# Performance work log

Hardware: AMD Instinct MI355X
Metric: run time of the kernel (lower is better)

## Reference

```python
import jax, jax.numpy as jnp
import numpy as np

N_E = 1024
E_DIM = 256
TAU = 0.5
BETA = 0.25
LAMB = 0.1
EPS = 1e-10


def setup_inputs() -> dict:
    key = jax.random.key(0)
    k1, k2, k3 = jax.random.split(key, 3)
    z = jax.random.normal(k1, (16, 1024, E_DIM), dtype=jnp.float32)
    # kaiming-normal-initialized codebook (std = sqrt(2 / fan_in))
    emb = jax.random.normal(k2, (N_E, E_DIM), dtype=jnp.float32) * np.sqrt(2.0 / E_DIM)
    u = jax.random.uniform(k3, (16 * 1024, N_E), dtype=jnp.float32)
    return {"z": z, "emb": emb, "u": u}


def reference(z, emb, u):
    zf = z.reshape(-1, E_DIM)                                  # [N, e_dim]
    # squared euclidean distances to each code: ||z||^2 + ||e||^2 - 2 z.e
    d = (jnp.sum(zf * zf, axis=1, keepdims=True)
         + jnp.sum(emb * emb, axis=1)
         - 2.0 * jnp.matmul(zf, emb.T))                        # [N, n_e]
    # gumbel-softmax (hard, straight-through) on logits = -d
    g = -jnp.log(-jnp.log(u + EPS) + EPS)
    y_soft = jax.nn.softmax((-d + g) / TAU, axis=-1)
    idx = jnp.argmax(y_soft, axis=-1)
    y_hard = jax.nn.one_hot(idx, N_E, dtype=y_soft.dtype)
    probs = y_hard + y_soft - jax.lax.stop_gradient(y_soft)    # [N, n_e]
    z_q = jnp.matmul(probs, emb).reshape(z.shape)
    # orthogonality loss on the codebook gram matrix
    gram = jnp.matmul(emb, emb.T)
    ortho = jnp.mean((gram - jnp.eye(N_E, dtype=emb.dtype)) ** 2) / (N_E ** 2)
    emb_loss = jnp.mean((jax.lax.stop_gradient(z_q) - z) ** 2)
    commit = BETA * jnp.mean((z_q - jax.lax.stop_gradient(z)) ** 2)
    loss = emb_loss + BETA * commit + LAMB * ortho
    z_q_st = z + jax.lax.stop_gradient(z_q - z)
    e_mean = jnp.mean(probs, axis=0)
    perplexity = jnp.exp(-jnp.sum(e_mean * jnp.log(e_mean + EPS)))
    return loss, z_q_st, perplexity
```

## Files before the change

### kernel.cpp

```cpp
#include <hip/hip_runtime.h>
#include <math.h>
#include <stdint.h>


#define NROWS 16384
#define NE    1024
#define ED    256
#define EPSF  1e-10f
#define INV2048 4.8828125e-4f
#define BK 64

typedef _Float16 half_t;
typedef __attribute__((ext_vector_type(4))) _Float16 half4;
typedef __attribute__((ext_vector_type(8))) _Float16 half8;
typedef __attribute__((ext_vector_type(16))) float floatx16;
typedef unsigned long long u64;

__device__ __forceinline__ void gl_lds16(const half_t* g, half_t* l) {
    __builtin_amdgcn_global_load_lds(
        (const __attribute__((address_space(1))) uint32_t*)g,
        (__attribute__((address_space(3))) uint32_t*)l, 16, 0, 0);
}

__device__ __forceinline__ u64 packMax(float v, int code) {
    unsigned int b   = __float_as_uint(v);
    unsigned int key = (b & 0x80000000u) ? ~b : (b | 0x80000000u);
    return ((u64)key << 32) | (unsigned int)(NE - 1 - code);
}

__global__ __launch_bounds__(256) void vq_prep(
        const float* __restrict__ z, const float* __restrict__ emb,
        half_t* __restrict__ zh, half_t* __restrict__ zl,
        half_t* __restrict__ eh, half_t* __restrict__ el,
        float* __restrict__ enorm, u64* __restrict__ best,
        int* __restrict__ cnt, double* __restrict__ mse_acc,
        int* __restrict__ done_cnt)
{
    const int gid = blockIdx.x * 256 + threadIdx.x;
    const int ZQ4 = NROWS * ED / 4;
    if (gid < ZQ4) {
        const float4 v = ((const float4*)z)[gid];
        const float x[4] = {v.x, v.y, v.z, v.w};
        half4 h, l;
#pragma unroll
        for (int i = 0; i < 4; ++i) {
            const half_t hi = (half_t)x[i];
            h[i] = hi; l[i] = (half_t)((x[i] - (float)hi) * 2048.0f);
        }
        *(half4*)&zh[(size_t)gid * 4] = h;
        *(half4*)&zl[(size_t)gid * 4] = l;
    } else {
        const int eg = gid - ZQ4;
        const float4 v = ((const float4*)emb)[eg];
        const float x[4] = {v.x, v.y, v.z, v.w};
        half4 h, l;
#pragma unroll
        for (int i = 0; i < 4; ++i) {
            const half_t hi = (half_t)x[i];
            h[i] = hi; l[i] = (half_t)((x[i] - (float)hi) * 2048.0f);
        }
        *(half4*)&eh[(size_t)eg * 4] = h;
        *(half4*)&el[(size_t)eg * 4] = l;
        float s = v.x*v.x + v.y*v.y + v.z*v.z + v.w*v.w;
#pragma unroll
        for (int o = 32; o; o >>= 1) s += __shfl_down(s, o);
        if ((threadIdx.x & 63) == 0) enorm[eg >> 6] = s;
        if (eg < NROWS) best[eg] = 0ull;
        if (eg < NE)    cnt[eg]  = 0;
        if (eg == 0)  { *mse_acc = 0.0; *done_cnt = 0; }
    }
}

#define SCW 132
__global__ __launch_bounds__(256, 2) void vq_gemm(
        const half_t* __restrict__ zh, const half_t* __restrict__ zl,
        const half_t* __restrict__ eh, const half_t* __restrict__ el,
        const float* __restrict__ u, const float* __restrict__ enorm,
        u64* __restrict__ best)
{
    __shared__ __align__(16) char smem[128 * SCW * 4 + 2048];
    half_t* Ah = (half_t*)smem;
    half_t* Al = (half_t*)(smem + 16384);
    half_t* Bh = (half_t*)(smem + 32768);
    half_t* Bl = (half_t*)(smem + 49152);
    float (*Sc)[SCW] = (float(*)[SCW])smem;
    u64* parr = (u64*)(smem + 128 * SCW * 4);

    const int t    = threadIdx.x;
    const int w    = t >> 6;
    const int lane = t & 63;
    const int m0 = blockIdx.x * 128, n0 = blockIdx.y * 128;
    const int wm = (w >> 1) * 64,    wn = (w & 1) * 64;
    const int lrow = lane & 31;
    const int hw   = lane >> 5;

    floatx16 accH[2][2] = {};
    floatx16 accX[2][2] = {};

    for (int kc = 0; kc < ED; kc += BK) {
        __syncthreads();
#pragma unroll
        for (int it = 0; it < 4; ++it) {
            const int s   = it * 256 + t;
            const int row = s >> 3;
            const int c   = (s & 7) ^ (row & 7);
            const int ldsoff = (it * 256 + w * 64) * 8;
            const size_t ga = (size_t)(m0 + row) * ED + kc + c * 8;
            const size_t gb = (size_t)(n0 + row) * ED + kc + c * 8;
            gl_lds16(zh + ga, Ah + ldsoff);
            gl_lds16(zl + ga, Al + ldsoff);
            gl_lds16(eh + gb, Bh + ldsoff);
            gl_lds16(el + gb, Bl + ldsoff);
        }
        __syncthreads();
#pragma unroll
        for (int ks = 0; ks < BK / 16; ++ks) {
            const int cch = ks * 2 + hw;
            half8 ah[2], al[2], bh[2], bl[2];
#pragma unroll
            for (int i = 0; i < 2; ++i) {
                const int ar = wm + i * 32 + lrow;
                const int br = wn + i * 32 + lrow;
                const int sa = ar * 8 + (cch ^ (ar & 7));
                const int sb = br * 8 + (cch ^ (br & 7));
                ah[i] = *(const half8*)&Ah[sa * 8];
                al[i] = *(const half8*)&Al[sa * 8];
                bh[i] = *(const half8*)&Bh[sb * 8];
                bl[i] = *(const half8*)&Bl[sb * 8];
            }
#pragma unroll
            for (int i = 0; i < 2; ++i)
#pragma unroll
            for (int j = 0; j < 2; ++j) {
                accH[i][j] = __builtin_amdgcn_mfma_f32_32x32x16_f16(ah[i], bh[j], accH[i][j], 0, 0, 0);
                accX[i][j] = __builtin_amdgcn_mfma_f32_32x32x16_f16(ah[i], bl[j], accX[i][j], 0, 0, 0);
                accX[i][j] = __builtin_amdgcn_mfma_f32_32x32x16_f16(al[i], bh[j], accX[i][j], 0, 0, 0);
            }
        }
    }
    __syncthreads();

    const int   col0 = n0 + wn + lrow;
    const float en0  = enorm[col0];
    const float en1  = enorm[col0 + 32];
#pragma unroll
    for (int i = 0; i < 2; ++i) {
#pragma unroll
        for (int r = 0; r < 16; ++r) {
            const int lr = wm + i * 32 + (r & 3) + ((r >> 2) << 3) + (hw << 2);
            const size_t urow = (size_t)(m0 + lr) * NE;
            const float d0 = accH[i][0][r] + accX[i][0][r] * INV2048;
            const float d1 = accH[i][1][r] + accX[i][1][r] * INV2048;
            const float g0 = -__logf(-__logf(u[urow + col0] + EPSF) + EPSF);
            const float g1 = -__logf(-__logf(u[urow + col0 + 32] + EPSF) + EPSF);
            Sc[lr][wn + lrow]      = 2.f * d0 - en0 + g0;
            Sc[lr][wn + lrow + 32] = 2.f * d1 - en1 + g1;
        }
    }
    __syncthreads();

    {
        const int row = t >> 1;
        const int ch  = (t & 1) << 6;
        float bv = -1e38f; int bc = 0;
#pragma unroll
        for (int q = 0; q < 16; ++q) {
            const float4 v = *(const float4*)&Sc[row][ch + (q << 2)];
            const int c = n0 + ch + (q << 2);
            if (v.x > bv) { bv = v.x; bc = c; }
            if (v.y > bv) { bv = v.y; bc = c + 1; }
            if (v.z > bv) { bv = v.z; bc = c + 2; }
            if (v.w > bv) { bv = v.w; bc = c + 3; }
        }
        parr[t] = packMax(bv, bc);
    }
    __syncthreads();
    if (t < 128) {
        const u64 a = parr[t << 1], b = parr[(t << 1) + 1];
        atomicMax(&best[m0 + t], a > b ? a : b);
    }
}

__global__ __launch_bounds__(256) void vq_outfin(
        const float* __restrict__ z, const float* __restrict__ emb,
        const u64* __restrict__ best, int* __restrict__ cnt,
        double* __restrict__ mse_acc, int* __restrict__ done_cnt,
        float* __restrict__ out)
{
    __shared__ int    ridx[64];
    __shared__ float  redf[4];
    __shared__ double redd[4];
    __shared__ int    flag;
    const int t  = threadIdx.x;
    const int m0 = blockIdx.x * 64;

    if (t < 64) {
        const u64 p = best[m0 + t];
        const int code = NE - 1 - (int)(p & 0xFFFFFFFFu);
        ridx[t] = code;
        atomicAdd(&cnt[code], 1);
    }
    __syncthreads();

    float lmse = 0.f;
#pragma unroll
    for (int rr = 0; rr < 16; ++rr) {
        const int row = (rr << 2) + (t >> 6);
        const int d4  = (t & 63) << 2;
        const int j   = ridx[row];
        const size_t zb = (size_t)(m0 + row) * ED;
        const float4 zv = *(const float4*)&z[zb + d4];
        const float4 ev = *(const float4*)&emb[(size_t)j * ED + d4];
        const float zz[4] = {zv.x, zv.y, zv.z, zv.w};
        const float ee[4] = {ev.x, ev.y, ev.z, ev.w};
#pragma unroll
        for (int q = 0; q < 4; ++q) {
            const float df = ee[q] - zz[q];
            out[1 + zb + d4 + q] = zz[q] + df;
            lmse = fmaf(df, df, lmse);
        }
    }
#pragma unroll
    for (int o = 32; o; o >>= 1) lmse += __shfl_down(lmse, o);
    if ((t & 63) == 0) redf[t >> 6] = lmse;
    __syncthreads();
    if (t == 0) {
        atomicAdd(mse_acc, (double)(redf[0] + redf[1] + redf[2] + redf[3]));
        __threadfence();
        flag = (atomicAdd(done_cnt, 1) == NROWS / 64 - 1) ? 1 : 0;
    }
    __syncthreads();
    if (flag) {
        double s = 0.0;
#pragma unroll
        for (int q = 0; q < 4; ++q) {
            const int   c  = atomicAdd(&cnt[(q << 8) + t], 0);
            const float em = (float)c / (float)NROWS;
            s += (double)(em * logf(em + EPSF));
        }
#pragma unroll
        for (int o = 32; o; o >>= 1) s += __shfl_down(s, o);
        if ((t & 63) == 0) redd[t >> 6] = s;
        __syncthreads();
        if (t == 0) {
            const double tot = redd[0] + redd[1] + redd[2] + redd[3];
            const double mse = atomicAdd(mse_acc, 0.0) / (double)((size_t)NROWS * ED);
            out[0] = (float)(mse * 1.0625);
            out[1 + (size_t)NROWS * ED] = (float)exp(-tot);
        }
    }
}

extern "C" void kernel_launch(void* const* d_in, const int* in_sizes, int n_in,
                              void* d_out, int out_size, void* d_ws, size_t ws_size,
                              hipStream_t stream) {
    const float* z   = (const float*)d_in[0];
    const float* emb = (const float*)d_in[1];
    const float* u   = (const float*)d_in[2];
    float* out = (float*)d_out;

    double* mse_acc  = (double*)d_ws;
    int*    done_cnt = (int*)((char*)d_ws + 64);
    int*    cnt      = (int*)((char*)d_ws + 1024);
    float*  enorm    = (float*)((char*)d_ws + 5120);
    u64*    best     = (u64*)((char*)d_ws + 9216);
    const size_t small_end = 140288;

    const size_t zsplit = (size_t)NROWS * ED * 2;
    const size_t esplit = (size_t)NE * ED * 2;
    const bool bigws = ws_size >= small_end + 2 * zsplit + 2 * esplit;

    half_t *zh, *zl, *eh, *el;
    if (bigws) {
        char* big = (char*)d_ws + small_end;
        zh = (half_t*)big;
        zl = (half_t*)(big + zsplit);
        eh = (half_t*)(big + 2 * zsplit);
        el = (half_t*)(big + 2 * zsplit + esplit);
    } else {
        zh = (half_t*)((char*)d_out + 8);
        zl = (half_t*)((char*)d_out + 8 + zsplit);
        eh = (half_t*)((char*)d_ws + small_end);
        el = (half_t*)((char*)d_ws + small_end + esplit);
    }

    vq_prep<<<(NROWS * ED / 4 + NE * ED / 4) / 256, 256, 0, stream>>>(
        z, emb, zh, zl, eh, el, enorm, best, cnt, mse_acc, done_cnt);
    vq_gemm<<<dim3(NROWS / 128, NE / 128), 256, 0, stream>>>(
        zh, zl, eh, el, u, enorm, best);
    vq_outfin<<<NROWS / 64, 256, 0, stream>>>(
        z, emb, best, cnt, mse_acc, done_cnt, out);
}
```

Measured before the change: 171.2 us.

## Restructure VQ GEMM to 512 threads with smaller K-tiles and phased LDS argmax

The distance GEMM now runs 8 waves per block, each computing a 64x32 sub-tile instead of 64x64, which halves the per-wave accumulators. The K step shrinks from 64 to 32 with a 4-chunk rotation swizzle, so LDS use drops to 32KB. That should allow more resident blocks per CU and better latency hiding. The gumbel and distance epilogue is applied in registers, and the row argmax is done in two LDS phases with shared-memory atomicMax, in place of a full 128x132 score tile. The output kernel also uses 32-row blocks for more parallelism, at the cost of more global atomics and more barriers per K loop.

```diff
diff --git a/kernel.cpp b/kernel.cpp
--- a/kernel.cpp
+++ b/kernel.cpp
@@ -8,7 +8,6 @@
 #define ED    256
 #define EPSF  1e-10f
 #define INV2048 4.8828125e-4f
-#define BK 64
 
 typedef _Float16 half_t;
 typedef __attribute__((ext_vector_type(4))) _Float16 half4;
@@ -71,130 +70,133 @@
     }
 }
 
-#define SCW 132
-__global__ __launch_bounds__(256, 2) void vq_gemm(
+__global__ __launch_bounds__(512, 4) void vq_gemm(
         const half_t* __restrict__ zh, const half_t* __restrict__ zl,
         const half_t* __restrict__ eh, const half_t* __restrict__ el,
         const float* __restrict__ u, const float* __restrict__ enorm,
         u64* __restrict__ best)
 {
-    __shared__ __align__(16) char smem[128 * SCW * 4 + 2048];
-    half_t* Ah = (half_t*)smem;
-    half_t* Al = (half_t*)(smem + 16384);
-    half_t* Bh = (half_t*)(smem + 32768);
-    half_t* Bl = (half_t*)(smem + 49152);
-    float (*Sc)[SCW] = (float(*)[SCW])smem;
-    u64* parr = (u64*)(smem + 128 * SCW * 4);
+    __shared__ __align__(16) half_t smem[4 * 4096];
+    __shared__ u64 bl[128];
+    half_t* Ah = smem;
+    half_t* Al = smem + 4096;
+    half_t* Bh = smem + 8192;
+    half_t* Bl = smem + 12288;
 
     const int t    = threadIdx.x;
     const int w    = t >> 6;
     const int lane = t & 63;
-    const int m0 = blockIdx.x * 128, n0 = blockIdx.y * 128;
-    const int wm = (w >> 1) * 64,    wn = (w & 1) * 64;
     const int lrow = lane & 31;
     const int hw   = lane >> 5;
-
-    floatx16 accH[2][2] = {};
-    floatx16 accX[2][2] = {};
-
-    for (int kc = 0; kc < ED; kc += BK) {
-        __syncthreads();
-#pragma unroll
-        for (int it = 0; it < 4; ++it) {
-            const int s   = it * 256 + t;
-            const int row = s >> 3;
-            const int c   = (s & 7) ^ (row & 7);
-            const int ldsoff = (it * 256 + w * 64) * 8;
-            const size_t ga = (size_t)(m0 + row) * ED + kc + c * 8;
-            const size_t gb = (size_t)(n0 + row) * ED + kc + c * 8;
-            gl_lds16(zh + ga, Ah + ldsoff);
-            gl_lds16(zl + ga, Al + ldsoff);
-            gl_lds16(eh + gb, Bh + ldsoff);
-            gl_lds16(el + gb, Bl + ldsoff);
-        }
-        __syncthreads();
-#pragma unroll
-        for (int ks = 0; ks < BK / 16; ++ks) {
+    const int m0 = blockIdx.x * 128, n0 = blockIdx.y * 128;
+    const int wm = (w & 1) * 64;
+    const int wn = (w >> 1) * 32;
+
+    if (t < 128) bl[t] = 0ull;
+
+    const int srow = t >> 2;
+    const int schunk = ((t & 3) - (srow >> 1)) & 3;
+    const size_t gaoff = (size_t)(m0 + srow) * ED + schunk * 8;
+    const size_t gboff = (size_t)(n0 + srow) * ED + schunk * 8;
+    const int ldsbase = w * 512;
+
+    floatx16 accH[2] = {};
+    floatx16 accX[2] = {};
+
+    for (int kc = 0; kc < ED; kc += 32) {
+        __syncthreads();
+        gl_lds16(zh + gaoff + kc, Ah + ldsbase);
+        gl_lds16(zl + gaoff + kc, Al + ldsbase);
+        gl_lds16(eh + gboff + kc, Bh + ldsbase);
+        gl_lds16(el + gboff + kc, Bl + ldsbase);
+        __syncthreads();
+#pragma unroll
+        for (int ks = 0; ks < 2; ++ks) {
             const int cch = ks * 2 + hw;
-            half8 ah[2], al[2], bh[2], bl[2];
+            half8 ah[2], al[2], bh, blo;
+            {
+                const int br = wn + lrow;
+                const int sb = br * 4 + ((cch + (br >> 1)) & 3);
+                bh  = *(const half8*)&Bh[sb * 8];
+                blo = *(const half8*)&Bl[sb * 8];
+            }
 #pragma unroll
             for (int i = 0; i < 2; ++i) {
                 const int ar = wm + i * 32 + lrow;
-                const int br = wn + i * 32 + lrow;
-                const int sa = ar * 8 + (cch ^ (ar & 7));
-                const int sb = br * 8 + (cch ^ (br & 7));
+                const int sa = ar * 4 + ((cch + (ar >> 1)) & 3);
                 ah[i] = *(const half8*)&Ah[sa * 8];
                 al[i] = *(const half8*)&Al[sa * 8];
-                bh[i] = *(const half8*)&Bh[sb * 8];
-                bl[i] = *(const half8*)&Bl[sb * 8];
-            }
-#pragma unroll
-            for (int i = 0; i < 2; ++i)
-#pragma unroll
-            for (int j = 0; j < 2; ++j) {
-                accH[i][j] = __builtin_amdgcn_mfma_f32_32x32x16_f16(ah[i], bh[j], accH[i][j], 0, 0, 0);
-                accX[i][j] = __builtin_amdgcn_mfma_f32_32x32x16_f16(ah[i], bl[j], accX[i][j], 0, 0, 0);
-                accX[i][j] = __builtin_amdgcn_mfma_f32_32x32x16_f16(al[i], bh[j], accX[i][j], 0, 0, 0);
-            }
-        }
-    }
-    __syncthreads();
+            }
+#pragma unroll
+            for (int i = 0; i < 2; ++i) {
+                accH[i] = __builtin_amdgcn_mfma_f32_32x32x16_f16(ah[i], bh,  accH[i], 0, 0, 0);
+                accX[i] = __builtin_amdgcn_mfma_f32_32x32x16_f16(ah[i], blo, accX[i], 0, 0, 0);
+                accX[i] = __builtin_amdgcn_mfma_f32_32x32x16_f16(al[i], bh,  accX[i], 0, 0, 0);
+            }
+        }
+    }
 
     const int   col0 = n0 + wn + lrow;
     const float en0  = enorm[col0];
-    const float en1  = enorm[col0 + 32];
-#pragma unroll
-    for (int i = 0; i < 2; ++i) {
+#pragma unroll
+    for (int i = 0; i < 2; ++i)
 #pragma unroll
         for (int r = 0; r < 16; ++r) {
             const int lr = wm + i * 32 + (r & 3) + ((r >> 2) << 3) + (hw << 2);
-            const size_t urow = (size_t)(m0 + lr) * NE;
-            const float d0 = accH[i][0][r] + accX[i][0][r] * INV2048;
-            const float d1 = accH[i][1][r] + accX[i][1][r] * INV2048;
-            const float g0 = -__logf(-__logf(u[urow + col0] + EPSF) + EPSF);
-            const float g1 = -__logf(-__logf(u[urow + col0 + 32] + EPSF) + EPSF);
-            Sc[lr][wn + lrow]      = 2.f * d0 - en0 + g0;
-            Sc[lr][wn + lrow + 32] = 2.f * d1 - en1 + g1;
-        }
-    }
-    __syncthreads();
-
-    {
-        const int row = t >> 1;
-        const int ch  = (t & 1) << 6;
-        float bv = -1e38f; int bc = 0;
-#pragma unroll
-        for (int q = 0; q < 16; ++q) {
-            const float4 v = *(const float4*)&Sc[row][ch + (q << 2)];
-            const int c = n0 + ch + (q << 2);
-            if (v.x > bv) { bv = v.x; bc = c; }
-            if (v.y > bv) { bv = v.y; bc = c + 1; }
-            if (v.z > bv) { bv = v.z; bc = c + 2; }
-            if (v.w > bv) { bv = v.w; bc = c + 3; }
-        }
-        parr[t] = packMax(bv, bc);
-    }
-    __syncthreads();
-    if (t < 128) {
-        const u64 a = parr[t << 1], b = parr[(t << 1) + 1];
-        atomicMax(&best[m0 + t], a > b ? a : b);
-    }
-}
-
+            const float uu = u[(size_t)(m0 + lr) * NE + col0];
+            const float g  = -__logf(-__logf(uu + EPSF) + EPSF);
+            accH[i][r] = 2.f * (accH[i][r] + accX[i][r] * INV2048) - en0 + g;
+        }
+
+    float (*Sc)[128] = (float(*)[128])smem;
+#pragma unroll
+    for (int ph = 0; ph < 2; ++ph) {
+        __syncthreads();
+        if ((w & 1) == ph) {
+#pragma unroll
+            for (int i = 0; i < 2; ++i)
+#pragma unroll
+                for (int r = 0; r < 16; ++r) {
+                    const int lr = i * 32 + (r & 3) + ((r >> 2) << 3) + (hw << 2);
+                    Sc[lr][wn + lrow] = accH[i][r];
+                }
+        }
+        __syncthreads();
+        {
+            const int row = t >> 3;
+            const int cb  = (t & 7) << 4;
+            float bv = -1e38f; int bc = 0;
+#pragma unroll
+            for (int q = 0; q < 4; ++q) {
+                const float4 v = *(const float4*)&Sc[row][cb + (q << 2)];
+                const int c = n0 + cb + (q << 2);
+                if (v.x > bv) { bv = v.x; bc = c; }
+                if (v.y > bv) { bv = v.y; bc = c + 1; }
+                if (v.z > bv) { bv = v.z; bc = c + 2; }
+                if (v.w > bv) { bv = v.w; bc = c + 3; }
+            }
+            atomicMax(&bl[ph * 64 + row], packMax(bv, bc));
+        }
+    }
+    __syncthreads();
+    if (t < 128) atomicMax(&best[m0 + t], bl[t]);
+}
+
+#define OB 32
 __global__ __launch_bounds__(256) void vq_outfin(
         const float* __restrict__ z, const float* __restrict__ emb,
         const u64* __restrict__ best, int* __restrict__ cnt,
         double* __restrict__ mse_acc, int* __restrict__ done_cnt,
         float* __restrict__ out)
 {
-    __shared__ int    ridx[64];
+    __shared__ int    ridx[OB];
     __shared__ float  redf[4];
     __shared__ double redd[4];
     __shared__ int    flag;
     const int t  = threadIdx.x;
-    const int m0 = blockIdx.x * 64;
-
-    if (t < 64) {
+    const int m0 = blockIdx.x * OB;
+
+    if (t < OB) {
         const u64 p = best[m0 + t];
         const int code = NE - 1 - (int)(p & 0xFFFFFFFFu);
         ridx[t] = code;
@@ -204,7 +206,7 @@
 
     float lmse = 0.f;
 #pragma unroll
-    for (int rr = 0; rr < 16; ++rr) {
+    for (int rr = 0; rr < OB / 4; ++rr) {
         const int row = (rr << 2) + (t >> 6);
         const int d4  = (t & 63) << 2;
         const int j   = ridx[row];
@@ -227,7 +229,7 @@
     if (t == 0) {
         atomicAdd(mse_acc, (double)(redf[0] + redf[1] + redf[2] + redf[3]));
         __threadfence();
-        flag = (atomicAdd(done_cnt, 1) == NROWS / 64 - 1) ? 1 : 0;
+        flag = (atomicAdd(done_cnt, 1) == NROWS / OB - 1) ? 1 : 0;
     }
     __syncthreads();
     if (flag) {
@@ -286,8 +288,8 @@
 
     vq_prep<<<(NROWS * ED / 4 + NE * ED / 4) / 256, 256, 0, stream>>>(
         z, emb, zh, zl, eh, el, enorm, best, cnt, mse_acc, done_cnt);
-    vq_gemm<<<dim3(NROWS / 128, NE / 128), 256, 0, stream>>>(
+    vq_gemm<<<dim3(NROWS / 128, NE / 128), 512, 0, stream>>>(
         zh, zl, eh, el, u, enorm, best);
-    vq_outfin<<<NROWS / 64, 256, 0, stream>>>(
+    vq_outfin<<<NROWS / OB, 256, 0, stream>>>(
         z, emb, best, cnt, mse_acc, done_cnt, out);
 }
```

Measured after the change: 186.1 us. 1.09x slower.
